# Kernel tuning notes

Measured on AMD Instinct MI355X. Metric: run time of the kernel, lower is better.

## Reference

```python
import jax, jax.numpy as jnp
import numpy as np

B, T, A, D = 256, 2048, 22, 2
MAX_GAP = 512  # max NaN-gap length injected per row


def setup_inputs() -> dict:
    key = jax.random.key(0)
    k1, k2, k3 = jax.random.split(key, 3)
    x = jax.random.normal(k1, (B, T, A, D), dtype=jnp.float32)
    # one contiguous NaN gap per row: frames (s, e) exclusive are NaN
    s = jax.random.randint(k2, (B,), 1, T // 2)        # last valid frame before gap
    gap = jax.random.randint(k3, (B,), 1, MAX_GAP)     # gap length
    e = s + gap + 1                                    # first valid frame after gap
    t = jnp.arange(T)
    gap_mask = (t[None, :] > s[:, None]) & (t[None, :] < e[:, None])  # [B, T]
    x = jnp.where(gap_mask[:, :, None, None], jnp.nan, x)
    return {"x": x}


def reference(x):
    # x: [B, T, A, D] with one contiguous NaN gap along T per row.
    Bn, Tn = x.shape[0], x.shape[1]
    nan_mask = jnp.isnan(x).reshape(Bn, Tn, -1).any(axis=2)       # [B, T]
    start = jnp.argmax(nan_mask, axis=1) - 1                       # last valid before gap
    end = Tn - jnp.argmax(nan_mask[:, ::-1], axis=1)               # first valid after gap

    b = jnp.arange(Bn)
    x_s = x[b, start]                                              # [B, A, D]
    x_e = x[b, end]                                                # [B, A, D]

    t = jnp.arange(Tn)[None, :]                                    # [1, T]
    # weight at frame t is (t - s) / (e - s), matching linspace(0,1,gap+2)[1:-1]
    w = (t - start[:, None]).astype(x.dtype) / (end - start)[:, None].astype(x.dtype)
    w = w[:, :, None, None]                                        # [B, T, 1, 1]
    interp = x_s[:, None] * (1.0 - w) + x_e[:, None] * w           # [B, T, A, D]

    in_gap = (t > start[:, None]) & (t < end[:, None])             # [B, T]
    return jnp.where(in_gap[:, :, None, None], interp, x)
```

## Files before the change

kernel.cpp:

```cpp
#include <hip/hip_runtime.h>

#define BB 256
#define TT 2048
#define AD 44
#define AD4 11
#define F4_PER_B (TT * AD4)
#define ELEMS 8
#define BLK_F4 (256 * ELEMS)
#define BLOCKS_PER_B 11
#define NCOPY (BB * BLOCKS_PER_B)
#define NBLK (BB + NCOPY)

typedef float v4 __attribute__((ext_vector_type(4)));

__device__ __forceinline__ void block_minmax(const int tid, int& tmin, int& tmax,
                                             int* smin, int* smax) {
#pragma unroll
  for (int d = 32; d > 0; d >>= 1) {
    tmin = min(tmin, __shfl_xor(tmin, d));
    tmax = max(tmax, __shfl_xor(tmax, d));
  }
  const int wid = tid >> 6;
  if ((tid & 63) == 0) { smin[wid] = tmin; smax[wid] = tmax; }
  __syncthreads();
  if (tid == 0) {
    int a = smin[0], z = smax[0];
#pragma unroll
    for (int i = 1; i < 4; ++i) { a = min(a, smin[i]); z = max(z, smax[i]); }
    smin[0] = a; smax[0] = z;
  }
  __syncthreads();
  tmin = smin[0];
  tmax = smax[0];
  __syncthreads();
}

__global__ __launch_bounds__(256) void interp_one(const v4* __restrict__ x4,
                                                  v4* __restrict__ out4) {
  const int tid = threadIdx.x;

  if (blockIdx.x >= BB) {
    const int cid = blockIdx.x - BB;
    const int b = cid / BLOCKS_PER_B;
    const int blk_in_b = cid - b * BLOCKS_PER_B;
    const size_t base = (size_t)b * F4_PER_B + (size_t)blk_in_b * BLK_F4;

    v4 v[ELEMS];
#pragma unroll
    for (int k = 0; k < ELEMS; ++k) {
      v[k] = x4[base + k * 256 + tid];
    }
#pragma unroll
    for (int k = 0; k < ELEMS; ++k) {
      const v4 w = v[k];
      const bool n = (w.x != w.x) || (w.y != w.y) || (w.z != w.z) || (w.w != w.w);
      if (!n) out4[base + k * 256 + tid] = w;
    }
    return;
  }

  const int b = blockIdx.x;
  const float* xf = (const float*)x4;
  const size_t fbase = (size_t)b * (TT * AD);
  __shared__ int smin[4], smax[4];

  int tmin = TT, tmax = -1;
  {
    const int r = tid * 8;
    const float c = xf[fbase + (size_t)r * AD];
    if (c != c) { tmin = r; tmax = r; }
  }
  block_minmax(tid, tmin, tmax, smin, smax);

  if (tmax < 0) {
    tmin = TT; tmax = -1;
#pragma unroll
    for (int k = 0; k < 8; ++k) {
      const int r = k * 256 + tid;
      const float c = xf[fbase + (size_t)r * AD];
      if (c != c) { tmin = min(tmin, r); tmax = max(tmax, r); }
    }
    block_minmax(tid, tmin, tmax, smin, smax);
  } else {
    const int cmin = tmin, cmax = tmax;
    tmin = cmin; tmax = cmax;
    if (tid < 7) {
      const int r = cmin - 1 - tid;
      if (r >= 0) { const float c = xf[fbase + (size_t)r * AD]; if (c != c) tmin = r; }
    } else if (tid >= 64 && tid < 71) {
      const int r = cmax + 1 + (tid - 64);
      if (r < TT) { const float c = xf[fbase + (size_t)r * AD]; if (c != c) tmax = r; }
    }
    block_minmax(tid, tmin, tmax, smin, smax);
  }

  int s, e;
  if (tmax < 0) {
    s = 0; e = 1;
  } else {
    s = tmin - 1;
    e = min(tmax + 1, TT - 1);
  }

  __shared__ v4 sxs[AD4], sxe[AD4];
  const size_t base = (size_t)b * F4_PER_B;
  if (tid < AD4) sxs[tid] = x4[base + (size_t)s * AD4 + tid];
  if (tid >= 64 && tid < 64 + AD4) sxe[tid - 64] = x4[base + (size_t)e * AD4 + (tid - 64)];
  __syncthreads();

  const float inv = 1.0f / (float)(e - s);
  const int total = (e - s - 1) * AD4;
  for (int i = tid; i < total; i += 256) {
    const int dt = i / AD4;
    const int cch = i - dt * AD4;
    const int t = s + 1 + dt;
    const float w = (float)(dt + 1) * inv;
    const float om = 1.0f - w;
    const v4 a = sxs[cch];
    const v4 z = sxe[cch];
    v4 r;
    r.x = a.x * om + z.x * w;
    r.y = a.y * om + z.y * w;
    r.z = a.z * om + z.z * w;
    r.w = a.w * om + z.w * w;
    out4[base + (size_t)t * AD4 + cch] = r;
  }
}

extern "C" void kernel_launch(void* const* d_in, const int* in_sizes, int n_in,
                              void* d_out, int out_size, void* d_ws, size_t ws_size,
                              hipStream_t stream) {
  const v4* x4 = (const v4*)d_in[0];
  v4* out4 = (v4*)d_out;
  interp_one<<<NBLK, 256, 0, stream>>>(x4, out4);
}
```

Before: 162.4 us.

## Fuse gap detection into every copy block and write all outputs uniformly

```diff
diff --git a/kernel.cpp b/kernel.cpp
--- a/kernel.cpp
+++ b/kernel.cpp
@@ -8,8 +8,7 @@
 #define ELEMS 8
 #define BLK_F4 (256 * ELEMS)
 #define BLOCKS_PER_B 11
-#define NCOPY (BB * BLOCKS_PER_B)
-#define NBLK (BB + NCOPY)
+#define NBLK (BB * BLOCKS_PER_B)
 
 typedef float v4 __attribute__((ext_vector_type(4)));
 
@@ -35,31 +34,24 @@
   __syncthreads();
 }
 
-__global__ __launch_bounds__(256) void interp_one(const v4* __restrict__ x4,
-                                                  v4* __restrict__ out4) {
+__global__ __launch_bounds__(256) void interp_v7(const v4* __restrict__ x4,
+                                                 v4* __restrict__ out4) {
   const int tid = threadIdx.x;
+  const int b = blockIdx.x / BLOCKS_PER_B;
+  const int blk_in_b = blockIdx.x - b * BLOCKS_PER_B;
+  const int base_in_b = blk_in_b * BLK_F4;
+  const size_t base = (size_t)b * F4_PER_B + base_in_b;
 
-  if (blockIdx.x >= BB) {
-    const int cid = blockIdx.x - BB;
-    const int b = cid / BLOCKS_PER_B;
-    const int blk_in_b = cid - b * BLOCKS_PER_B;
-    const size_t base = (size_t)b * F4_PER_B + (size_t)blk_in_b * BLK_F4;
-
-    v4 v[ELEMS];
+  const v4* bp = x4 + base;
+  v4 d[ELEMS];
 #pragma unroll
-    for (int k = 0; k < ELEMS; ++k) {
-      v[k] = x4[base + k * 256 + tid];
-    }
-#pragma unroll
-    for (int k = 0; k < ELEMS; ++k) {
-      const v4 w = v[k];
-      const bool n = (w.x != w.x) || (w.y != w.y) || (w.z != w.z) || (w.w != w.w);
-      if (!n) out4[base + k * 256 + tid] = w;
-    }
-    return;
+  for (int k = 0; k < ELEMS; ++k) {
+    const unsigned off = (unsigned)((k * 256 + tid) * 16);
+    asm volatile("global_load_dwordx4 %0, %1, %2 offset:0"
+                 : "=v"(d[k])
+                 : "v"(off), "s"(bp));
   }
 
-  const int b = blockIdx.x;
   const float* xf = (const float*)x4;
   const size_t fbase = (size_t)b * (TT * AD);
   __shared__ int smin[4], smax[4];
@@ -103,27 +95,31 @@
   }
 
   __shared__ v4 sxs[AD4], sxe[AD4];
-  const size_t base = (size_t)b * F4_PER_B;
-  if (tid < AD4) sxs[tid] = x4[base + (size_t)s * AD4 + tid];
-  if (tid >= 64 && tid < 64 + AD4) sxe[tid - 64] = x4[base + (size_t)e * AD4 + (tid - 64)];
+  const size_t batch_base = (size_t)b * F4_PER_B;
+  if (tid < AD4) sxs[tid] = x4[batch_base + (size_t)s * AD4 + tid];
+  if (tid >= 64 && tid < 64 + AD4) sxe[tid - 64] = x4[batch_base + (size_t)e * AD4 + (tid - 64)];
   __syncthreads();
 
+  asm volatile("s_waitcnt vmcnt(0)" ::: "memory");
+  __builtin_amdgcn_sched_barrier(0);
+
   const float inv = 1.0f / (float)(e - s);
-  const int total = (e - s - 1) * AD4;
-  for (int i = tid; i < total; i += 256) {
-    const int dt = i / AD4;
-    const int cch = i - dt * AD4;
-    const int t = s + 1 + dt;
-    const float w = (float)(dt + 1) * inv;
+#pragma unroll
+  for (int k = 0; k < ELEMS; ++k) {
+    const int idx = base_in_b + k * 256 + tid;
+    const int t = idx / AD4;
+    const int c = idx - t * AD4;
+    const bool g = (t > s) && (t < e);
+    const float w = (float)(t - s) * inv;
     const float om = 1.0f - w;
-    const v4 a = sxs[cch];
-    const v4 z = sxe[cch];
+    const v4 a = sxs[c];
+    const v4 z = sxe[c];
     v4 r;
-    r.x = a.x * om + z.x * w;
-    r.y = a.y * om + z.y * w;
-    r.z = a.z * om + z.z * w;
-    r.w = a.w * om + z.w * w;
-    out4[base + (size_t)t * AD4 + cch] = r;
+    r.x = g ? (a.x * om + z.x * w) : d[k].x;
+    r.y = g ? (a.y * om + z.y * w) : d[k].y;
+    r.z = g ? (a.z * om + z.z * w) : d[k].z;
+    r.w = g ? (a.w * om + z.w * w) : d[k].w;
+    out4[base + k * 256 + tid] = r;
   }
 }
 
@@ -132,5 +128,5 @@
                               hipStream_t stream) {
   const v4* x4 = (const v4*)d_in[0];
   v4* out4 = (v4*)d_out;
-  interp_one<<<NBLK, 256, 0, stream>>>(x4, out4);
+  interp_v7<<<NBLK, 256, 0, stream>>>(x4, out4);
 }
```

New measurement: 163.8 us. No clear change (+0.8%).
